# Kernel tuning notes

Hardware: AMD Instinct MI355X
Metric: run time of the kernel (lower is better)

The kernel has to match this reference:

```python
import jax, jax.numpy as jnp
import numpy as np

KH = KW = 3
SH = SW = 1
DH = DW = 1

def _same_padding(ih, iw):
    eff_kh = (KH - 1) * DH + 1
    eff_kw = (KW - 1) * DW + 1
    out_h = (ih + SH - 1) // SH
    out_w = (iw + SW - 1) // SW
    pad_h = max((out_h - 1) * SH + eff_kh - ih, 0)
    pad_w = max((out_w - 1) * SW + eff_kw - iw, 0)
    pad_top = pad_h // 2
    pad_bottom = pad_h - pad_top
    pad_left = pad_w // 2
    pad_right = pad_w - pad_left
    return (pad_top, pad_bottom), (pad_left, pad_right)


def setup_inputs() -> dict:
    key = jax.random.key(0)
    k1, k2, k3 = jax.random.split(key, 3)
    N, C, H, Wd = 32, 192, 56, 56
    Cout = 384
    x = jax.random.normal(k1, (N, C, H, Wd), dtype=jnp.float32)
    # linear weight (Cout, C*KH*KW) with unfold ordering (c, kh, kw) -> OIHW kernel
    W = jax.random.normal(k2, (Cout, C, KH, KW), dtype=jnp.float32) * (1.0 / np.sqrt(C * KH * KW))
    b = jax.random.normal(k3, (Cout,), dtype=jnp.float32) * 0.01
    return {"x": x, "W": W, "b": b}


def reference(x, W, b):
    # ConvLayer: F.pad('same') -> nn.Unfold -> Linear -> reshape, which is
    # mathematically a 2D conv with OIHW kernel W (unfold orders features as c,kh,kw).
    _, _, H, Wd = x.shape
    pad_hw = _same_padding(H, Wd)
    out = jax.lax.conv_general_dilated(
        x, W,
        window_strides=(SH, SW),
        padding=pad_hw,
        rhs_dilation=(DH, DW),
        dimension_numbers=("NCHW", "OIHW", "NCHW"),
    )
    return out + b[None, :, None, None]
```

## Files before the change

### kernel.cpp

```cpp
#include <hip/hip_runtime.h>
#include <cstdint>
#include <cstddef>

#define N_IMG 32
#define C_IN 192
#define HW 56
#define SPAT 3136
#define C_OUT 384
#define HP 58
#define KPOS 9
#define KTOT 1728
#define NT 27

#define BM 128
#define BN 256
#define NT_CO 3
#define NT_S  392
#define GRID_MAIN (NT_CO*NT_S)

#define BUF_EL 24576
#define B_BASE 8192

typedef __attribute__((ext_vector_type(8))) short short8;
typedef __attribute__((ext_vector_type(4))) float f32x4;

__device__ __forceinline__ unsigned short f2bf(float f) {
  union { float f; unsigned u; } v; v.f = f;
  unsigned u = v.u;
  unsigned r = (u + 0x7FFFu + ((u >> 16) & 1u)) >> 16;
  return (unsigned short)r;
}

__device__ __forceinline__ void async_load16(const void* gsrc, void* ldst) {
  __builtin_amdgcn_global_load_lds(
      (const __attribute__((address_space(1))) unsigned int*)gsrc,
      (__attribute__((address_space(3))) unsigned int*)ldst,
      16, 0, 0);
}

__device__ __forceinline__ void vm6() { asm volatile("s_waitcnt vmcnt(6)" ::: "memory"); }
__device__ __forceinline__ void vm0() { asm volatile("s_waitcnt vmcnt(0)" ::: "memory"); }

__global__ void pack_w(const float* __restrict__ W, unsigned short* __restrict__ Wp) {
  int idx = blockIdx.x*256 + threadIdx.x;
  if (idx >= C_OUT*KPOS*C_IN) return;
  int c   = idx % C_IN;
  int pos = (idx / C_IN) % KPOS;
  int co  = idx / (C_IN*KPOS);
  float v = W[((size_t)co*C_IN + c)*KPOS + pos];
  Wp[idx] = f2bf(v);
}

__global__ void zero_border(unsigned short* __restrict__ Xp) {
  int idx = blockIdx.x*256 + threadIdx.x;
  if (idx >= N_IMG*228*C_IN) return;
  int c    = idx % C_IN;
  int cell = (idx / C_IN) % 228;
  int n    = idx / (C_IN*228);
  int hh, ww;
  if (cell < 116) { hh = (cell < 58) ? 0 : 57; ww = cell % 58; }
  else { int b2 = cell - 116; ww = (b2 < 56) ? 0 : 57; hh = 1 + (b2 % 56); }
  Xp[(((size_t)n*HP + hh)*HP + ww)*C_IN + c] = 0;
}

__global__ void pack_x(const float* __restrict__ x, unsigned short* __restrict__ Xp) {
  __shared__ float tile[64*57];
  int b  = blockIdx.x;
  int cb = b % 3;
  int h  = (b/3) % HW;
  int n  = b / (3*HW);
  int tid = threadIdx.x;
  const float* src = x + (size_t)n*C_IN*SPAT + (size_t)cb*64*SPAT + h*HW;
  #pragma unroll
  for (int i = 0; i < 14; ++i) {
    int idx = i*256 + tid;
    int c = idx / HW, w = idx % HW;
    tile[c*57 + w] = src[(size_t)c*SPAT + w];
  }
  __syncthreads();
  unsigned short* dst = Xp + (((size_t)n*HP + h + 1)*HP + 1)*C_IN + cb*64;
  #pragma unroll
  for (int i = 0; i < 14; ++i) {
    int idx = i*256 + tid;
    int w = idx / 64, c = idx % 64;
    dst[(size_t)w*C_IN + c] = f2bf(tile[c*57 + w]);
  }
}

__global__ __launch_bounds__(512, 2) void conv_gemm(
    const unsigned short* __restrict__ Wp,
    const unsigned short* __restrict__ Xp,
    const float* __restrict__ bias,
    float* __restrict__ out)
{
  __shared__ __attribute__((aligned(16))) unsigned short lds[3][BUF_EL];

  int bid = blockIdx.x;
  int wg = (bid & 7) * (GRID_MAIN/8) + (bid >> 3);
  int cotile = wg % NT_CO;
  int stile  = wg / NT_CO;

  const int tid   = threadIdx.x;
  const int lane  = tid & 63;
  const int wv    = tid >> 6;
  const int wm    = wv >> 2;
  const int wn    = wv & 3;
  const int lanep = lane & 15;
  const int laneq = lane >> 4;
  const int l3    = lane >> 3;
  const int l7    = lane & 7;
  const int gsl   = (l7 ^ l3) << 3;

  const unsigned short* aSrc0 = Wp + (size_t)(cotile*BM + wv*8      + l3)*KTOT + gsl;
  const unsigned short* aSrc1 = Wp + (size_t)(cotile*BM + (wv+8)*8  + l3)*KTOT + gsl;
  const int aOff0 = wv*512;
  const int aOff1 = (wv+8)*512;

  const unsigned short* bSrc[4];
  int bOff[4];
  #pragma unroll
  for (int i = 0; i < 4; ++i) {
    int cbk = i*8 + wv;
    int rb  = cbk*8 + l3;
    int f   = stile*BN + rb;
    int n   = f / SPAT, sp = f % SPAT;
    bSrc[i] = Xp + (((size_t)n*HP + sp/HW)*HP + sp%HW)*C_IN + gsl;
    bOff[i] = B_BASE + cbk*512;
  }

  const int aRd = (wm*64 + lanep)*64 + ((laneq ^ (lanep & 7)) << 3);
  const int bRd = B_BASE + (wn*64 + lanep)*64 + ((laneq ^ (lanep & 7)) << 3);

  f32x4 acc[4][4];
  #pragma unroll
  for (int mf = 0; mf < 4; ++mf)
    #pragma unroll
    for (int nf = 0; nf < 4; ++nf)
      acc[mf][nf] = (f32x4){0.f, 0.f, 0.f, 0.f};

  auto bOffOf = [](int t) {
    int pos = t / 3;
    int c0  = (t - pos*3) * 64;
    int kh  = pos / 3, kw = pos - kh*3;
    return (kh*HP + kw)*C_IN + c0;
  };

  auto stage = [&](int t, unsigned short* base) {
    const int koff = t*64;
    async_load16(aSrc0 + koff, base + aOff0);
    async_load16(aSrc1 + koff, base + aOff1);
    const int bo = bOffOf(t);
    #pragma unroll
    for (int i = 0; i < 4; ++i)
      async_load16(bSrc[i] + bo, base + bOff[i]);
  };

#define PHASE(LB, STAGE_STMT, VM_STMT, DO_BAR)                              \
  {                                                                         \
    const unsigned short* lb_ = (LB);                                       \
    short8 a0_[4], b0_[4], a1_[4], b1_[4];                                  \
    _Pragma("unroll")                                                       \
    for (int mf = 0; mf < 4; ++mf) a0_[mf] = *(const short8*)&lb_[aRd + mf*1024];        \
    _Pragma("unroll")                                                       \
    for (int nf = 0; nf < 4; ++nf) b0_[nf] = *(const short8*)&lb_[bRd + nf*1024];        \
    _Pragma("unroll")                                                       \
    for (int mf = 0; mf < 4; ++mf) a1_[mf] = *(const short8*)&lb_[(aRd + mf*1024) ^ 32]; \
    _Pragma("unroll")                                                       \
    for (int nf = 0; nf < 4; ++nf) b1_[nf] = *(const short8*)&lb_[(bRd + nf*1024) ^ 32]; \
    STAGE_STMT;                                                             \
    __builtin_amdgcn_s_setprio(1);                                          \
    _Pragma("unroll")                                                       \
    for (int mf = 0; mf < 4; ++mf)                                          \
      _Pragma("unroll")                                                     \
      for (int nf = 0; nf < 4; ++nf)                                        \
        acc[mf][nf] = __builtin_amdgcn_mfma_f32_16x16x32_bf16(              \
            a0_[mf], b0_[nf], acc[mf][nf], 0, 0, 0);                        \
    _Pragma("unroll")                                                       \
    for (int mf = 0; mf < 4; ++mf)                                          \
      _Pragma("unroll")                                                     \
      for (int nf = 0; nf < 4; ++nf)                                        \
        acc[mf][nf] = __builtin_amdgcn_mfma_f32_16x16x32_bf16(              \
            a1_[mf], b1_[nf], acc[mf][nf], 0, 0, 0);                        \
    __builtin_amdgcn_s_setprio(0);                                          \
    VM_STMT;                                                                \
    if (DO_BAR) {                                                           \
      __builtin_amdgcn_s_barrier();                                         \
      __builtin_amdgcn_sched_barrier(0);                                    \
    }                                                                       \
  }

  unsigned short* b0 = &lds[0][0];
  unsigned short* b1 = &lds[1][0];
  unsigned short* b2 = &lds[2][0];

  stage(0, b0);
  stage(1, b1);
  vm6();
  __builtin_amdgcn_s_barrier();
  __builtin_amdgcn_sched_barrier(0);

  for (int t0 = 0; t0 < 24; t0 += 3) {
    PHASE(b0, { stage(t0 + 2, b2); }, vm6(), true);
    PHASE(b1, { stage(t0 + 3, b0); }, vm6(), true);
    PHASE(b2, { stage(t0 + 4, b1); }, vm6(), true);
  }
  PHASE(b0, { stage(26, b2); }, vm6(), true);
  PHASE(b1, {}, vm0(), true);
  PHASE(b2, {}, {}, false);
#undef PHASE

  const int coB = cotile*BM + wm*64;
  const int fB  = stile*BN + wn*64;
  #pragma unroll
  for (int nf = 0; nf < 4; ++nf) {
    int f  = fB + nf*16 + lanep;
    int n  = f / SPAT;
    int sp = f % SPAT;
    float* obase = out + (size_t)n*C_OUT*SPAT + sp;
    #pragma unroll
    for (int mf = 0; mf < 4; ++mf) {
      #pragma unroll
      for (int i = 0; i < 4; ++i) {
        int co = coB + mf*16 + laneq*4 + i;
        obase[(size_t)co*SPAT] = acc[mf][nf][i] + bias[co];
      }
    }
  }
}

__global__ void conv_naive(const float* __restrict__ x, const float* __restrict__ W,
                           const float* __restrict__ bias, float* __restrict__ out) {
  size_t idx = (size_t)blockIdx.x*256 + threadIdx.x;
  if (idx >= (size_t)N_IMG*C_OUT*SPAT) return;
  int s  = idx % SPAT;
  int co = (int)((idx / SPAT) % C_OUT);
  int n  = (int)(idx / ((size_t)SPAT*C_OUT));
  int h = s / HW, w = s % HW;
  float acc = bias[co];
  for (int c = 0; c < C_IN; ++c)
    for (int kh = 0; kh < 3; ++kh) {
      int hh = h + kh - 1;
      if (hh < 0 || hh >= HW) continue;
      for (int kw = 0; kw < 3; ++kw) {
        int ww = w + kw - 1;
        if (ww < 0 || ww >= HW) continue;
        acc += x[(((size_t)n*C_IN + c)*HW + hh)*HW + ww]
             * W[(((size_t)co*C_IN + c)*3 + kh)*3 + kw];
      }
    }
  out[idx] = acc;
}

extern "C" void kernel_launch(void* const* d_in, const int* in_sizes, int n_in,
                              void* d_out, int out_size, void* d_ws, size_t ws_size,
                              hipStream_t stream) {
  const float* x = (const float*)d_in[0];
  const float* W = (const float*)d_in[1];
  const float* b = (const float*)d_in[2];
  float* out = (float*)d_out;

  const size_t WP_ELEMS = (size_t)C_OUT*KPOS*C_IN;
  const size_t XP_ELEMS = (size_t)N_IMG*HP*HP*C_IN;
  const size_t NEED = (WP_ELEMS + XP_ELEMS)*2;

  if (ws_size >= NEED) {
    unsigned short* Wp = (unsigned short*)d_ws;
    unsigned short* Xp = Wp + WP_ELEMS;
    zero_border<<<(N_IMG*228*C_IN + 255)/256, 256, 0, stream>>>(Xp);
    pack_w<<<(int)((WP_ELEMS + 255)/256), 256, 0, stream>>>(W, Wp);
    pack_x<<<N_IMG*HW*3, 256, 0, stream>>>(x, Xp);
    conv_gemm<<<GRID_MAIN, 512, 0, stream>>>(Wp, Xp, b, out);
  } else {
    size_t total = (size_t)N_IMG*C_OUT*SPAT;
    conv_naive<<<(int)((total + 255)/256), 256, 0, stream>>>(x, W, b, out);
  }
}
```

Measured before the change: 166.3 us.

## Load weight fragments directly into registers from fragment-packed layout, bypassing LDS

Weights are pre-packed into an MFMA-fragment-ordered layout so each lane can load its A operands straight from global memory into registers. These loads are double-buffered one k-step ahead, and only the input tile goes through LDS. This cuts LDS traffic and footprint (buffer shrinks from 24K to 16K elements) and removes the A-side ds_reads. In exchange it uses more VGPRs for two A register sets, and it relies on global/L2 latency being hidden within one phase.

```diff
diff --git a/kernel.cpp b/kernel.cpp
--- a/kernel.cpp
+++ b/kernel.cpp
@@ -18,8 +18,7 @@
 #define NT_S  392
 #define GRID_MAIN (NT_CO*NT_S)
 
-#define BUF_EL 24576
-#define B_BASE 8192
+#define BUF_EL 16384
 
 typedef __attribute__((ext_vector_type(8))) short short8;
 typedef __attribute__((ext_vector_type(4))) float f32x4;
@@ -38,17 +37,23 @@
       16, 0, 0);
 }
 
-__device__ __forceinline__ void vm6() { asm volatile("s_waitcnt vmcnt(6)" ::: "memory"); }
+__device__ __forceinline__ void vm4() { asm volatile("s_waitcnt vmcnt(4)" ::: "memory"); }
 __device__ __forceinline__ void vm0() { asm volatile("s_waitcnt vmcnt(0)" ::: "memory"); }
-
-__global__ void pack_w(const float* __restrict__ W, unsigned short* __restrict__ Wp) {
+#define SBAR0() __builtin_amdgcn_sched_barrier(0)
+
+__global__ void pack_w(const float* __restrict__ W, unsigned short* __restrict__ WpF) {
   int idx = blockIdx.x*256 + threadIdx.x;
-  if (idx >= C_OUT*KPOS*C_IN) return;
-  int c   = idx % C_IN;
-  int pos = (idx / C_IN) % KPOS;
-  int co  = idx / (C_IN*KPOS);
+  if (idx >= C_OUT*KTOT) return;
+  int co = idx / KTOT;
+  int k  = idx % KTOT;
+  int pos = k / C_IN;
+  int c   = k % C_IN;
   float v = W[((size_t)co*C_IN + c)*KPOS + pos];
-  Wp[idx] = f2bf(v);
+  int mb = co >> 4, r = co & 15;
+  int kb = k >> 5,  cc = k & 31;
+  int l  = r + ((cc >> 3) << 4);
+  int j  = cc & 7;
+  WpF[((size_t)mb*54 + kb)*512 + l*8 + j] = f2bf(v);
 }
 
 __global__ void zero_border(unsigned short* __restrict__ Xp) {
@@ -88,7 +93,7 @@
 }
 
 __global__ __launch_bounds__(512, 2) void conv_gemm(
-    const unsigned short* __restrict__ Wp,
+    const unsigned short* __restrict__ WpF,
     const unsigned short* __restrict__ Xp,
     const float* __restrict__ bias,
     float* __restrict__ out)
@@ -111,10 +116,10 @@
   const int l7    = lane & 7;
   const int gsl   = (l7 ^ l3) << 3;
 
-  const unsigned short* aSrc0 = Wp + (size_t)(cotile*BM + wv*8      + l3)*KTOT + gsl;
-  const unsigned short* aSrc1 = Wp + (size_t)(cotile*BM + (wv+8)*8  + l3)*KTOT + gsl;
-  const int aOff0 = wv*512;
-  const int aOff1 = (wv+8)*512;
+  const short8* aP[4];
+  #pragma unroll
+  for (int mf = 0; mf < 4; ++mf)
+    aP[mf] = ((const short8*)WpF) + ((size_t)(cotile*8 + wm*4 + mf)*54)*64 + lane;
 
   const unsigned short* bSrc[4];
   int bOff[4];
@@ -125,11 +130,10 @@
     int f   = stile*BN + rb;
     int n   = f / SPAT, sp = f % SPAT;
     bSrc[i] = Xp + (((size_t)n*HP + sp/HW)*HP + sp%HW)*C_IN + gsl;
-    bOff[i] = B_BASE + cbk*512;
-  }
-
-  const int aRd = (wm*64 + lanep)*64 + ((laneq ^ (lanep & 7)) << 3);
-  const int bRd = B_BASE + (wn*64 + lanep)*64 + ((laneq ^ (lanep & 7)) << 3);
+    bOff[i] = cbk*512;
+  }
+
+  const int bRd = (wn*64 + lanep)*64 + ((laneq ^ (lanep & 7)) << 3);
 
   f32x4 acc[4][4];
   #pragma unroll
@@ -146,46 +150,51 @@
   };
 
   auto stage = [&](int t, unsigned short* base) {
-    const int koff = t*64;
-    async_load16(aSrc0 + koff, base + aOff0);
-    async_load16(aSrc1 + koff, base + aOff1);
     const int bo = bOffOf(t);
     #pragma unroll
     for (int i = 0; i < 4; ++i)
       async_load16(bSrc[i] + bo, base + bOff[i]);
   };
 
-#define PHASE(LB, STAGE_STMT, VM_STMT, DO_BAR)                              \
+  short8 aA[8], aB[8];
+
+#define PHASE(LB, AC, AN, DO_PREF, T1, STAGE_STMT, VM_STMT, DO_BAR)         \
   {                                                                         \
     const unsigned short* lb_ = (LB);                                       \
-    short8 a0_[4], b0_[4], a1_[4], b1_[4];                                  \
-    _Pragma("unroll")                                                       \
-    for (int mf = 0; mf < 4; ++mf) a0_[mf] = *(const short8*)&lb_[aRd + mf*1024];        \
-    _Pragma("unroll")                                                       \
-    for (int nf = 0; nf < 4; ++nf) b0_[nf] = *(const short8*)&lb_[bRd + nf*1024];        \
-    _Pragma("unroll")                                                       \
-    for (int mf = 0; mf < 4; ++mf) a1_[mf] = *(const short8*)&lb_[(aRd + mf*1024) ^ 32]; \
-    _Pragma("unroll")                                                       \
-    for (int nf = 0; nf < 4; ++nf) b1_[nf] = *(const short8*)&lb_[(bRd + nf*1024) ^ 32]; \
+    short8 bv0_[4], bv1_[4];                                                \
+    _Pragma("unroll")                                                       \
+    for (int nf = 0; nf < 4; ++nf) bv0_[nf] = *(const short8*)&lb_[bRd + nf*1024];        \
+    _Pragma("unroll")                                                       \
+    for (int nf = 0; nf < 4; ++nf) bv1_[nf] = *(const short8*)&lb_[(bRd + nf*1024) ^ 32]; \
+    if (DO_PREF) {                                                          \
+      _Pragma("unroll")                                                     \
+      for (int kk = 0; kk < 2; ++kk)                                        \
+        _Pragma("unroll")                                                   \
+        for (int mf = 0; mf < 4; ++mf)                                      \
+          AN[kk*4+mf] = aP[mf][(2*(T1)+kk)*64];                             \
+    }                                                                       \
+    SBAR0();                                                                \
     STAGE_STMT;                                                             \
+    SBAR0();                                                                \
     __builtin_amdgcn_s_setprio(1);                                          \
     _Pragma("unroll")                                                       \
     for (int mf = 0; mf < 4; ++mf)                                          \
       _Pragma("unroll")                                                     \
       for (int nf = 0; nf < 4; ++nf)                                        \
         acc[mf][nf] = __builtin_amdgcn_mfma_f32_16x16x32_bf16(              \
-            a0_[mf], b0_[nf], acc[mf][nf], 0, 0, 0);                        \
+            AC[mf], bv0_[nf], acc[mf][nf], 0, 0, 0);                        \
     _Pragma("unroll")                                                       \
     for (int mf = 0; mf < 4; ++mf)                                          \
       _Pragma("unroll")                                                     \
       for (int nf = 0; nf < 4; ++nf)                                        \
         acc[mf][nf] = __builtin_amdgcn_mfma_f32_16x16x32_bf16(              \
-            a1_[mf], b1_[nf], acc[mf][nf], 0, 0, 0);                        \
+            AC[4+mf], bv1_[nf], acc[mf][nf], 0, 0, 0);                      \
     __builtin_amdgcn_s_setprio(0);                                          \
+    SBAR0();                                                                \
     VM_STMT;                                                                \
     if (DO_BAR) {                                                           \
       __builtin_amdgcn_s_barrier();                                         \
-      __builtin_amdgcn_sched_barrier(0);                                    \
+      SBAR0();                                                              \
     }                                                                       \
   }
 
@@ -193,20 +202,30 @@
   unsigned short* b1 = &lds[1][0];
   unsigned short* b2 = &lds[2][0];
 
+  #pragma unroll
+  for (int kk = 0; kk < 2; ++kk)
+    #pragma unroll
+    for (int mf = 0; mf < 4; ++mf)
+      aA[kk*4+mf] = aP[mf][kk*64];
+  SBAR0();
   stage(0, b0);
   stage(1, b1);
-  vm6();
+  SBAR0();
+  vm4();
   __builtin_amdgcn_s_barrier();
-  __builtin_amdgcn_sched_barrier(0);
-
-  for (int t0 = 0; t0 < 24; t0 += 3) {
-    PHASE(b0, { stage(t0 + 2, b2); }, vm6(), true);
-    PHASE(b1, { stage(t0 + 3, b0); }, vm6(), true);
-    PHASE(b2, { stage(t0 + 4, b1); }, vm6(), true);
-  }
-  PHASE(b0, { stage(26, b2); }, vm6(), true);
-  PHASE(b1, {}, vm0(), true);
-  PHASE(b2, {}, {}, false);
+  SBAR0();
+
+  for (int t0 = 0; t0 < 24; t0 += 6) {
+    PHASE(b0, aA, aB, true, t0+1, { stage(t0+2, b2); }, vm4(), true);
+    PHASE(b1, aB, aA, true, t0+2, { stage(t0+3, b0); }, vm4(), true);
+    PHASE(b2, aA, aB, true, t0+3, { stage(t0+4, b1); }, vm4(), true);
+    PHASE(b0, aB, aA, true, t0+4, { stage(t0+5, b2); }, vm4(), true);
+    PHASE(b1, aA, aB, true, t0+5, { stage(t0+6, b0); }, vm4(), true);
+    PHASE(b2, aB, aA, true, t0+6, { stage(t0+7, b1); }, vm4(), true);
+  }
+  PHASE(b0, aA, aB, true, 25, { stage(26, b2); }, vm4(), true);
+  PHASE(b1, aB, aA, true, 26, {}, vm0(), true);
+  PHASE(b2, aA, aB, false, 0, {}, {}, false);
 #undef PHASE
 
   const int coB = cotile*BM + wm*64;
@@ -259,17 +278,17 @@
   const float* b = (const float*)d_in[2];
   float* out = (float*)d_out;
 
-  const size_t WP_ELEMS = (size_t)C_OUT*KPOS*C_IN;
+  const size_t WP_ELEMS = (size_t)C_OUT*KTOT;
   const size_t XP_ELEMS = (size_t)N_IMG*HP*HP*C_IN;
   const size_t NEED = (WP_ELEMS + XP_ELEMS)*2;
 
   if (ws_size >= NEED) {
-    unsigned short* Wp = (unsigned short*)d_ws;
-    unsigned short* Xp = Wp + WP_ELEMS;
+    unsigned short* WpF = (unsigned short*)d_ws;
+    unsigned short* Xp  = WpF + WP_ELEMS;
     zero_border<<<(N_IMG*228*C_IN + 255)/256, 256, 0, stream>>>(Xp);
-    pack_w<<<(int)((WP_ELEMS + 255)/256), 256, 0, stream>>>(W, Wp);
+    pack_w<<<(int)((WP_ELEMS + 255)/256), 256, 0, stream>>>(W, WpF);
     pack_x<<<N_IMG*HW*3, 256, 0, stream>>>(x, Xp);
-    conv_gemm<<<GRID_MAIN, 512, 0, stream>>>(Wp, Xp, b, out);
+    conv_gemm<<<GRID_MAIN, 512, 0, stream>>>(WpF, Xp, b, out);
   } else {
     size_t total = (size_t)N_IMG*C_OUT*SPAT;
     conv_naive<<<(int)((total + 255)/256), 256, 0, stream>>>(x, W, b, out);
```

Result: slower. 204.7 us (+23.1%).

## Halve K-step to 32 to shrink LDS buffers and double occupancy

Applied to the files above, without the earlier changes.

The GEMM K-step per pipeline stage goes from 64 to 32, so each of the three LDS buffers holds half as much data and there are 54 phases instead of 27. The load mapping, swizzle pattern and wait counts are rewritten to match, and launch bounds ask for 4 blocks per CU instead of 2. The aim is higher occupancy to hide latency. In exchange there are twice as many barriers and fewer MFMAs between each sync.

```diff
diff --git a/kernel.cpp b/kernel.cpp
--- a/kernel.cpp
+++ b/kernel.cpp
@@ -10,7 +10,7 @@
 #define HP 58
 #define KPOS 9
 #define KTOT 1728
-#define NT 27
+#define NPH 54
 
 #define BM 128
 #define BN 256
@@ -18,8 +18,8 @@
 #define NT_S  392
 #define GRID_MAIN (NT_CO*NT_S)
 
-#define BUF_EL 24576
-#define B_BASE 8192
+#define BUF_EL 12288
+#define B_BASE 4096
 
 typedef __attribute__((ext_vector_type(8))) short short8;
 typedef __attribute__((ext_vector_type(4))) float f32x4;
@@ -38,8 +38,9 @@
       16, 0, 0);
 }
 
-__device__ __forceinline__ void vm6() { asm volatile("s_waitcnt vmcnt(6)" ::: "memory"); }
+__device__ __forceinline__ void vm3() { asm volatile("s_waitcnt vmcnt(3)" ::: "memory"); }
 __device__ __forceinline__ void vm0() { asm volatile("s_waitcnt vmcnt(0)" ::: "memory"); }
+#define SBAR0() __builtin_amdgcn_sched_barrier(0)
 
 __global__ void pack_w(const float* __restrict__ W, unsigned short* __restrict__ Wp) {
   int idx = blockIdx.x*256 + threadIdx.x;
@@ -87,7 +88,7 @@
   }
 }
 
-__global__ __launch_bounds__(512, 2) void conv_gemm(
+__global__ __launch_bounds__(512, 4) void conv_gemm(
     const unsigned short* __restrict__ Wp,
     const unsigned short* __restrict__ Xp,
     const float* __restrict__ bias,
@@ -107,29 +108,25 @@
   const int wn    = wv & 3;
   const int lanep = lane & 15;
   const int laneq = lane >> 4;
-  const int l3    = lane >> 3;
-  const int l7    = lane & 7;
-  const int gsl   = (l7 ^ l3) << 3;
-
-  const unsigned short* aSrc0 = Wp + (size_t)(cotile*BM + wv*8      + l3)*KTOT + gsl;
-  const unsigned short* aSrc1 = Wp + (size_t)(cotile*BM + (wv+8)*8  + l3)*KTOT + gsl;
-  const int aOff0 = wv*512;
-  const int aOff1 = (wv+8)*512;
-
-  const unsigned short* bSrc[4];
-  int bOff[4];
-  #pragma unroll
-  for (int i = 0; i < 4; ++i) {
-    int cbk = i*8 + wv;
-    int rb  = cbk*8 + l3;
-    int f   = stile*BN + rb;
-    int n   = f / SPAT, sp = f % SPAT;
-    bSrc[i] = Xp + (((size_t)n*HP + sp/HW)*HP + sp%HW)*C_IN + gsl;
-    bOff[i] = B_BASE + cbk*512;
-  }
-
-  const int aRd = (wm*64 + lanep)*64 + ((laneq ^ (lanep & 7)) << 3);
-  const int bRd = B_BASE + (wn*64 + lanep)*64 + ((laneq ^ (lanep & 7)) << 3);
+  const int r4    = (lane >> 2) & 15;
+  const int c4    = lane & 3;
+  const int gsl   = (c4 ^ ((r4 >> 1) & 3)) << 3;
+
+  const unsigned short* aSrc = Wp + (size_t)(cotile*BM + wv*16 + r4)*KTOT + gsl;
+  const unsigned short* bSrc0;
+  const unsigned short* bSrc1;
+  {
+    int f0 = stile*BN + (wv*2 + 0)*16 + r4;
+    int n0 = f0 / SPAT, sp0 = f0 % SPAT;
+    bSrc0 = Xp + (((size_t)n0*HP + sp0/HW)*HP + sp0%HW)*C_IN + gsl;
+    int f1 = stile*BN + (wv*2 + 1)*16 + r4;
+    int n1 = f1 / SPAT, sp1 = f1 % SPAT;
+    bSrc1 = Xp + (((size_t)n1*HP + sp1/HW)*HP + sp1%HW)*C_IN + gsl;
+  }
+
+  const int rsw = (laneq ^ ((lanep >> 1) & 3)) << 3;
+  const int aRd = (wm*64 + lanep)*32 + rsw;
+  const int bRd = B_BASE + (wn*64 + lanep)*32 + rsw;
 
   f32x4 acc[4][4];
   #pragma unroll
@@ -138,35 +135,24 @@
     for (int nf = 0; nf < 4; ++nf)
       acc[mf][nf] = (f32x4){0.f, 0.f, 0.f, 0.f};
 
-  auto bOffOf = [](int t) {
-    int pos = t / 3;
-    int c0  = (t - pos*3) * 64;
+  auto stage = [&](int t, unsigned short* base) {
+    int pos = t / 6;
+    int c0  = (t - pos*6) * 32;
     int kh  = pos / 3, kw = pos - kh*3;
-    return (kh*HP + kw)*C_IN + c0;
-  };
-
-  auto stage = [&](int t, unsigned short* base) {
-    const int koff = t*64;
-    async_load16(aSrc0 + koff, base + aOff0);
-    async_load16(aSrc1 + koff, base + aOff1);
-    const int bo = bOffOf(t);
-    #pragma unroll
-    for (int i = 0; i < 4; ++i)
-      async_load16(bSrc[i] + bo, base + bOff[i]);
+    int bo  = (kh*HP + kw)*C_IN + c0;
+    async_load16(aSrc + t*32, base + wv*512);
+    async_load16(bSrc0 + bo, base + B_BASE + (wv*2 + 0)*512);
+    async_load16(bSrc1 + bo, base + B_BASE + (wv*2 + 1)*512);
   };
 
 #define PHASE(LB, STAGE_STMT, VM_STMT, DO_BAR)                              \
   {                                                                         \
     const unsigned short* lb_ = (LB);                                       \
-    short8 a0_[4], b0_[4], a1_[4], b1_[4];                                  \
+    short8 av_[4], bv_[4];                                                  \
     _Pragma("unroll")                                                       \
-    for (int mf = 0; mf < 4; ++mf) a0_[mf] = *(const short8*)&lb_[aRd + mf*1024];        \
+    for (int mf = 0; mf < 4; ++mf) av_[mf] = *(const short8*)&lb_[aRd + mf*512]; \
     _Pragma("unroll")                                                       \
-    for (int nf = 0; nf < 4; ++nf) b0_[nf] = *(const short8*)&lb_[bRd + nf*1024];        \
-    _Pragma("unroll")                                                       \
-    for (int mf = 0; mf < 4; ++mf) a1_[mf] = *(const short8*)&lb_[(aRd + mf*1024) ^ 32]; \
-    _Pragma("unroll")                                                       \
-    for (int nf = 0; nf < 4; ++nf) b1_[nf] = *(const short8*)&lb_[(bRd + nf*1024) ^ 32]; \
+    for (int nf = 0; nf < 4; ++nf) bv_[nf] = *(const short8*)&lb_[bRd + nf*512]; \
     STAGE_STMT;                                                             \
     __builtin_amdgcn_s_setprio(1);                                          \
     _Pragma("unroll")                                                       \
@@ -174,18 +160,12 @@
       _Pragma("unroll")                                                     \
       for (int nf = 0; nf < 4; ++nf)                                        \
         acc[mf][nf] = __builtin_amdgcn_mfma_f32_16x16x32_bf16(              \
-            a0_[mf], b0_[nf], acc[mf][nf], 0, 0, 0);                        \
-    _Pragma("unroll")                                                       \
-    for (int mf = 0; mf < 4; ++mf)                                          \
-      _Pragma("unroll")                                                     \
-      for (int nf = 0; nf < 4; ++nf)                                        \
-        acc[mf][nf] = __builtin_amdgcn_mfma_f32_16x16x32_bf16(              \
-            a1_[mf], b1_[nf], acc[mf][nf], 0, 0, 0);                        \
+            av_[mf], bv_[nf], acc[mf][nf], 0, 0, 0);                        \
     __builtin_amdgcn_s_setprio(0);                                          \
     VM_STMT;                                                                \
     if (DO_BAR) {                                                           \
       __builtin_amdgcn_s_barrier();                                         \
-      __builtin_amdgcn_sched_barrier(0);                                    \
+      SBAR0();                                                              \
     }                                                                       \
   }
 
@@ -195,18 +175,18 @@
 
   stage(0, b0);
   stage(1, b1);
-  vm6();
+  vm3();
   __builtin_amdgcn_s_barrier();
-  __builtin_amdgcn_sched_barrier(0);
-
-  for (int t0 = 0; t0 < 24; t0 += 3) {
-    PHASE(b0, { stage(t0 + 2, b2); }, vm6(), true);
-    PHASE(b1, { stage(t0 + 3, b0); }, vm6(), true);
-    PHASE(b2, { stage(t0 + 4, b1); }, vm6(), true);
-  }
-  PHASE(b0, { stage(26, b2); }, vm6(), true);
-  PHASE(b1, {}, vm0(), true);
-  PHASE(b2, {}, {}, false);
+  SBAR0();
+
+  for (int t0 = 0; t0 < 51; t0 += 3) {
+    PHASE(b0, (stage(t0 + 2, b2)), vm3(), true);
+    PHASE(b1, (stage(t0 + 3, b0)), vm3(), true);
+    PHASE(b2, (stage(t0 + 4, b1)), vm3(), true);
+  }
+  PHASE(b0, (stage(53, b2)), vm3(), true);
+  PHASE(b1, (void)0, vm0(), true);
+  PHASE(b2, (void)0, (void)0, false);
 #undef PHASE
 
   const int coB = cotile*BM + wm*64;
@@ -259,7 +239,7 @@
   const float* b = (const float*)d_in[2];
   float* out = (float*)d_out;
 
-  const size_t WP_ELEMS = (size_t)C_OUT*KPOS*C_IN;
+  const size_t WP_ELEMS = (size_t)C_OUT*KTOT;
   const size_t XP_ELEMS = (size_t)N_IMG*HP*HP*C_IN;
   const size_t NEED = (WP_ELEMS + XP_ELEMS)*2;
 
```

Measured after the change: 172.2 us. 3.6% more time.

## Prefetch next tile's first k-half LDS fragments into registers across phases

Applied to the files above, without the earlier changes.

Restructures the main loop so each phase loads the first k-half of the next LDS buffer's A/B fragments into a register double buffer (pA0/pA1, pB0/pB1), while reading only the second half of the current buffer. This hides LDS read latency behind the MFMAs. Because the next buffer is now read a phase earlier, the partial vmcnt(6) wait is replaced by a full vmcnt(0) before every barrier. That shortens how far ahead the global-to-LDS loads can run and adds register pressure. The loop is unrolled by six to rotate the register buffers.

```diff
diff --git a/kernel.cpp b/kernel.cpp
--- a/kernel.cpp
+++ b/kernel.cpp
@@ -38,8 +38,8 @@
       16, 0, 0);
 }
 
-__device__ __forceinline__ void vm6() { asm volatile("s_waitcnt vmcnt(6)" ::: "memory"); }
 __device__ __forceinline__ void vm0() { asm volatile("s_waitcnt vmcnt(0)" ::: "memory"); }
+#define SBAR0() __builtin_amdgcn_sched_barrier(0)
 
 __global__ void pack_w(const float* __restrict__ W, unsigned short* __restrict__ Wp) {
   int idx = blockIdx.x*256 + threadIdx.x;
@@ -155,26 +155,32 @@
       async_load16(bSrc[i] + bo, base + bOff[i]);
   };
 
-#define PHASE(LB, STAGE_STMT, VM_STMT, DO_BAR)                              \
+  short8 pA0[4], pB0[4], pA1[4], pB1[4];
+
+#define PHASE(BC, BNX, RCA, RCB, RNA, RNB, DO_NEXT, STAGE_STMT, DO_BAR)     \
   {                                                                         \
-    const unsigned short* lb_ = (LB);                                       \
-    short8 a0_[4], b0_[4], a1_[4], b1_[4];                                  \
-    _Pragma("unroll")                                                       \
-    for (int mf = 0; mf < 4; ++mf) a0_[mf] = *(const short8*)&lb_[aRd + mf*1024];        \
-    _Pragma("unroll")                                                       \
-    for (int nf = 0; nf < 4; ++nf) b0_[nf] = *(const short8*)&lb_[bRd + nf*1024];        \
-    _Pragma("unroll")                                                       \
-    for (int mf = 0; mf < 4; ++mf) a1_[mf] = *(const short8*)&lb_[(aRd + mf*1024) ^ 32]; \
-    _Pragma("unroll")                                                       \
-    for (int nf = 0; nf < 4; ++nf) b1_[nf] = *(const short8*)&lb_[(bRd + nf*1024) ^ 32]; \
+    const unsigned short* bc_ = (BC);                                       \
+    const unsigned short* bn_ = (BNX);                                      \
+    short8 a1_[4], b1_[4];                                                  \
+    _Pragma("unroll")                                                       \
+    for (int mf = 0; mf < 4; ++mf) a1_[mf] = *(const short8*)&bc_[(aRd + mf*1024) ^ 32]; \
+    _Pragma("unroll")                                                       \
+    for (int nf = 0; nf < 4; ++nf) b1_[nf] = *(const short8*)&bc_[(bRd + nf*1024) ^ 32]; \
+    if (DO_NEXT) {                                                          \
+      _Pragma("unroll")                                                     \
+      for (int mf = 0; mf < 4; ++mf) RNA[mf] = *(const short8*)&bn_[aRd + mf*1024]; \
+      _Pragma("unroll")                                                     \
+      for (int nf = 0; nf < 4; ++nf) RNB[nf] = *(const short8*)&bn_[bRd + nf*1024]; \
+    }                                                                       \
     STAGE_STMT;                                                             \
+    SBAR0();                                                                \
     __builtin_amdgcn_s_setprio(1);                                          \
     _Pragma("unroll")                                                       \
     for (int mf = 0; mf < 4; ++mf)                                          \
       _Pragma("unroll")                                                     \
       for (int nf = 0; nf < 4; ++nf)                                        \
         acc[mf][nf] = __builtin_amdgcn_mfma_f32_16x16x32_bf16(              \
-            a0_[mf], b0_[nf], acc[mf][nf], 0, 0, 0);                        \
+            RCA[mf], RCB[nf], acc[mf][nf], 0, 0, 0);                        \
     _Pragma("unroll")                                                       \
     for (int mf = 0; mf < 4; ++mf)                                          \
       _Pragma("unroll")                                                     \
@@ -182,10 +188,11 @@
         acc[mf][nf] = __builtin_amdgcn_mfma_f32_16x16x32_bf16(              \
             a1_[mf], b1_[nf], acc[mf][nf], 0, 0, 0);                        \
     __builtin_amdgcn_s_setprio(0);                                          \
-    VM_STMT;                                                                \
+    SBAR0();                                                                \
     if (DO_BAR) {                                                           \
+      vm0();                                                                \
       __builtin_amdgcn_s_barrier();                                         \
-      __builtin_amdgcn_sched_barrier(0);                                    \
+      SBAR0();                                                              \
     }                                                                       \
   }
 
@@ -195,18 +202,25 @@
 
   stage(0, b0);
   stage(1, b1);
-  vm6();
+  vm0();
   __builtin_amdgcn_s_barrier();
-  __builtin_amdgcn_sched_barrier(0);
-
-  for (int t0 = 0; t0 < 24; t0 += 3) {
-    PHASE(b0, { stage(t0 + 2, b2); }, vm6(), true);
-    PHASE(b1, { stage(t0 + 3, b0); }, vm6(), true);
-    PHASE(b2, { stage(t0 + 4, b1); }, vm6(), true);
-  }
-  PHASE(b0, { stage(26, b2); }, vm6(), true);
-  PHASE(b1, {}, vm0(), true);
-  PHASE(b2, {}, {}, false);
+  SBAR0();
+  #pragma unroll
+  for (int mf = 0; mf < 4; ++mf) pA0[mf] = *(const short8*)&b0[aRd + mf*1024];
+  #pragma unroll
+  for (int nf = 0; nf < 4; ++nf) pB0[nf] = *(const short8*)&b0[bRd + nf*1024];
+
+  for (int t0 = 0; t0 < 24; t0 += 6) {
+    PHASE(b0, b1, pA0, pB0, pA1, pB1, true, (stage(t0 + 2, b2)), true);
+    PHASE(b1, b2, pA1, pB1, pA0, pB0, true, (stage(t0 + 3, b0)), true);
+    PHASE(b2, b0, pA0, pB0, pA1, pB1, true, (stage(t0 + 4, b1)), true);
+    PHASE(b0, b1, pA1, pB1, pA0, pB0, true, (stage(t0 + 5, b2)), true);
+    PHASE(b1, b2, pA0, pB0, pA1, pB1, true, (stage(t0 + 6, b0)), true);
+    PHASE(b2, b0, pA1, pB1, pA0, pB0, true, (stage(t0 + 7, b1)), true);
+  }
+  PHASE(b0, b1, pA0, pB0, pA1, pB1, true, (stage(26, b2)), true);
+  PHASE(b1, b2, pA1, pB1, pA0, pB0, true, (void)0, true);
+  PHASE(b2, b0, pA0, pB0, pA1, pB1, false, (void)0, false);
 #undef PHASE
 
   const int coB = cotile*BM + wm*64;
@@ -259,7 +273,7 @@
   const float* b = (const float*)d_in[2];
   float* out = (float*)d_out;
 
-  const size_t WP_ELEMS = (size_t)C_OUT*KPOS*C_IN;
+  const size_t WP_ELEMS = (size_t)C_OUT*KTOT;
   const size_t XP_ELEMS = (size_t)N_IMG*HP*HP*C_IN;
   const size_t NEED = (WP_ELEMS + XP_ELEMS)*2;
 
```

Result: slower. 169.7 us (+2.0%).
